# Kernel tuning notes

Hardware: AMD Instinct MI355X
Metric: run time of the kernel (lower is better)

Reference implementation:

```python
import jax, jax.numpy as jnp
import numpy as np

T, B, D, H = 2048, 8, 1024, 1024

def setup_inputs() -> dict:
    key = jax.random.key(0)
    k1, k2, k3 = jax.random.split(key, 3)
    std = 1.0 / H ** 0.5
    return {
        "x": jax.random.normal(k1, (T, B, D), dtype=jnp.float32),
        "h0": jnp.zeros((B, H), dtype=jnp.float32),
        "W_delta": jax.random.uniform(k2, (H, D), dtype=jnp.float32, minval=-0.1 * std, maxval=0.1 * std),
        "b_delta": jnp.full((H,), -1.8, dtype=jnp.float32),
        "W_B": jax.random.uniform(k3, (H, D), dtype=jnp.float32, minval=-std, maxval=std),
        "b_B": jnp.zeros((H,), dtype=jnp.float32),
    }

def reference(x, h0, W_delta, b_delta, W_B, b_B):
    # Projections over all T*B tokens at once (large GEMMs)
    delta = jax.nn.softplus(jnp.einsum('tbd,hd->tbh', x, W_delta) + b_delta)  # [T,B,H]
    decay = jnp.exp(-delta)                                                   # in (0,1)
    Bx = jnp.einsum('tbd,hd->tbh', x, W_B) + b_B                              # [T,B,H]
    # Sequential selective-decay linear recurrence: h = decay*h + (1-decay)*Bx
    def step(h, inp):
        a, bx = inp
        h_new = a * h + (1.0 - a) * bx
        return h_new, h_new
    _, hs = jax.lax.scan(step, h0, (decay, Bx))
    return hs  # [T,B,H]
```

## Files before the change

kernel.cpp:

```cpp
#include <hip/hip_runtime.h>
#include <hip/hip_bf16.h>

#define T_DIM 2048
#define B_DIM 8
#define D_DIM 1024
#define H_DIM 1024
#define M_DIM (T_DIM * B_DIM)
#define NCH (B_DIM * H_DIM)
#define CHUNK 64
#define NCHUNK (T_DIM / CHUNK)
#define NCH2 (NCH / 2)

typedef __bf16 bf16x8 __attribute__((ext_vector_type(8)));
typedef unsigned short us8 __attribute__((ext_vector_type(8)));
typedef float f32x4 __attribute__((ext_vector_type(4)));

__device__ __forceinline__ unsigned short f2bf(float f) {
    unsigned u = __float_as_uint(f);
    u += 0x7fffu + ((u >> 16) & 1u);
    return (unsigned short)(u >> 16);
}
__device__ __forceinline__ float bflo(unsigned u) { return __uint_as_float(u << 16); }
__device__ __forceinline__ float bfhi(unsigned u) { return __uint_as_float(u & 0xffff0000u); }

#define XCELLS  (M_DIM * D_DIM / 8)
#define WCELLS  (H_DIM * D_DIM / 8)
__global__ __launch_bounds__(256) void convert_kernel(
    const float* __restrict__ x, const float* __restrict__ Wd,
    const float* __restrict__ Wb, unsigned short* __restrict__ xb,
    unsigned short* __restrict__ wdb, unsigned short* __restrict__ wbb)
{
    size_t cell = (size_t)blockIdx.x * 256 + threadIdx.x;
    const float* src; unsigned short* dst;
    if (cell < XCELLS)               { src = x  + cell * 8;                    dst = xb  + cell * 8; }
    else if (cell < XCELLS + WCELLS) { size_t c = cell - XCELLS;  src = Wd + c * 8; dst = wdb + c * 8; }
    else                             { size_t c = cell - XCELLS - WCELLS; src = Wb + c * 8; dst = wbb + c * 8; }
    float4 f0 = *(const float4*)src;
    float4 f1 = *(const float4*)(src + 4);
    us8 u;
    u[0]=f2bf(f0.x); u[1]=f2bf(f0.y); u[2]=f2bf(f0.z); u[3]=f2bf(f0.w);
    u[4]=f2bf(f1.x); u[5]=f2bf(f1.y); u[6]=f2bf(f1.z); u[7]=f2bf(f1.w);
    *(us8*)dst = u;
}

__global__ __launch_bounds__(512, 2) void proj_kernel(
    const unsigned short* __restrict__ xb, const unsigned short* __restrict__ wdb,
    const unsigned short* __restrict__ wbb, const float* __restrict__ bd,
    const float* __restrict__ bb, unsigned int* __restrict__ db)
{
    __shared__ us8 lds[2][3072];

    const int tid  = threadIdx.x;
    const int lane = tid & 63;
    const int wid  = tid >> 6;
    const int wm = wid >> 2, wn = wid & 3;
    const int bRow = blockIdx.x * 128;
    const int bCol = blockIdx.y * 128;

    f32x4 accD[4][2], accB[4][2];
    #pragma unroll
    for (int i = 0; i < 4; ++i)
        #pragma unroll
        for (int j = 0; j < 2; ++j) { accD[i][j] = (f32x4)0.0f; accB[i][j] = (f32x4)0.0f; }

    const unsigned short* aBase  = xb  + (size_t)bRow * D_DIM;
    const unsigned short* b0Base = wdb + (size_t)bCol * D_DIM;
    const unsigned short* b1Base = wbb + (size_t)bCol * D_DIM;

    auto stage = [&](int buf, int kt) {
        #pragma unroll
        for (int p = 0; p < 6; ++p) {
            const unsigned short* base = (p < 2) ? aBase : (p < 4 ? b0Base : b1Base);
            int woff = (p & 1) * 512 + wid * 64;
            int w    = woff + lane;
            int row  = w >> 3;
            int kc   = (w & 7) ^ (row & 7);
            __builtin_amdgcn_global_load_lds(
                (const __attribute__((address_space(1))) unsigned int*)
                    (base + (size_t)row * D_DIM + kt + kc * 8),
                (__attribute__((address_space(3))) unsigned int*)
                    (&lds[buf][(p >> 1) * 1024 + woff]),
                16, 0, 0);
        }
    };

    auto compute = [&](int buf) {
        #pragma unroll
        for (int ks = 0; ks < 2; ++ks) {
            const int kc = ks * 4 + (lane >> 4);
            const int sl = kc ^ (lane & 7);
            bf16x8 aF[4], b0F[2], b1F[2];
            #pragma unroll
            for (int mt = 0; mt < 4; ++mt) {
                int r = wm * 64 + mt * 16 + (lane & 15);
                aF[mt] = __builtin_bit_cast(bf16x8, lds[buf][r * 8 + sl]);
            }
            #pragma unroll
            for (int nt = 0; nt < 2; ++nt) {
                int c = wn * 32 + nt * 16 + (lane & 15);
                b0F[nt] = __builtin_bit_cast(bf16x8, lds[buf][1024 + c * 8 + sl]);
                b1F[nt] = __builtin_bit_cast(bf16x8, lds[buf][2048 + c * 8 + sl]);
            }
            #pragma unroll
            for (int nt = 0; nt < 2; ++nt)
                #pragma unroll
                for (int mt = 0; mt < 4; ++mt) {
                    accD[mt][nt] = __builtin_amdgcn_mfma_f32_16x16x32_bf16(aF[mt], b0F[nt], accD[mt][nt], 0, 0, 0);
                    accB[mt][nt] = __builtin_amdgcn_mfma_f32_16x16x32_bf16(aF[mt], b1F[nt], accB[mt][nt], 0, 0, 0);
                }
        }
    };

    stage(0, 0);
    __syncthreads();
    for (int t = 0; t < 15; ++t) {
        stage((t + 1) & 1, (t + 1) * 64);
        compute(t & 1);
        __syncthreads();
    }
    compute(1);

    #pragma unroll
    for (int nt = 0; nt < 2; ++nt) {
        int c = bCol + wn * 32 + nt * 16 + (lane & 15);
        float bdv = bd[c], bbv = bb[c];
        #pragma unroll
        for (int mt = 0; mt < 4; ++mt) {
            int r0 = bRow + wm * 64 + mt * 16 + ((lane >> 4) << 2);
            #pragma unroll
            for (int reg = 0; reg < 4; ++reg) {
                float z  = accD[mt][nt][reg] + bdv;
                float dk = 1.0f / (1.0f + __expf(z));
                float bx = accB[mt][nt][reg] + bbv;
                db[(size_t)(r0 + reg) * H_DIM + c] =
                    (unsigned)f2bf(dk) | ((unsigned)f2bf(bx) << 16);
            }
        }
    }
}

__global__ __launch_bounds__(256) void scan_reduce(
    const uint2* __restrict__ db2, float2* __restrict__ cA, float2* __restrict__ cB)
{
    int c2 = blockIdx.y * 256 + threadIdx.x;
    int i  = blockIdx.x;
    const uint2* p = db2 + (size_t)i * CHUNK * NCH2 + c2;
    float A0 = 1.0f, B0 = 0.0f, A1 = 1.0f, B1 = 0.0f;
    for (int t = 0; t < CHUNK; ++t) {
        uint2 u = p[(size_t)t * NCH2];
        float a0 = bflo(u.x), bx0 = bfhi(u.x);
        float a1 = bflo(u.y), bx1 = bfhi(u.y);
        A0 *= a0; B0 = a0 * B0 + (1.0f - a0) * bx0;
        A1 *= a1; B1 = a1 * B1 + (1.0f - a1) * bx1;
    }
    cA[i * NCH2 + c2] = make_float2(A0, A1);
    cB[i * NCH2 + c2] = make_float2(B0, B1);
}

__global__ __launch_bounds__(256) void scan_chunks(
    const float2* __restrict__ cA, const float2* __restrict__ cB,
    const float2* __restrict__ h0, float2* __restrict__ hstart)
{
    int c2 = blockIdx.x * 256 + threadIdx.x;
    float2 h = h0[c2];
    #pragma unroll
    for (int i = 0; i < NCHUNK; ++i) {
        hstart[i * NCH2 + c2] = h;
        float2 a = cA[i * NCH2 + c2];
        float2 b = cB[i * NCH2 + c2];
        h.x = a.x * h.x + b.x;
        h.y = a.y * h.y + b.y;
    }
}

__global__ __launch_bounds__(256) void scan_apply(
    const uint2* __restrict__ db2, const float2* __restrict__ hstart,
    float2* __restrict__ out2)
{
    int c2 = blockIdx.y * 256 + threadIdx.x;
    int i  = blockIdx.x;
    float2 h = hstart[i * NCH2 + c2];
    const uint2* p = db2 + (size_t)i * CHUNK * NCH2 + c2;
    float2*      o = out2 + (size_t)i * CHUNK * NCH2 + c2;
    for (int t = 0; t < CHUNK; ++t) {
        uint2 u = p[(size_t)t * NCH2];
        float a0 = bflo(u.x), bx0 = bfhi(u.x);
        float a1 = bflo(u.y), bx1 = bfhi(u.y);
        h.x = a0 * h.x + (1.0f - a0) * bx0;
        h.y = a1 * h.y + (1.0f - a1) * bx1;
        o[(size_t)t * NCH2] = h;
    }
}

extern "C" void kernel_launch(void* const* d_in, const int* in_sizes, int n_in,
                              void* d_out, int out_size, void* d_ws, size_t ws_size,
                              hipStream_t stream) {
    const float* x  = (const float*)d_in[0];
    const float* h0 = (const float*)d_in[1];
    const float* Wd = (const float*)d_in[2];
    const float* bd = (const float*)d_in[3];
    const float* Wb = (const float*)d_in[4];
    const float* bb = (const float*)d_in[5];
    float* out = (float*)d_out;

    char* ws = (char*)d_ws;
    unsigned int* db = (unsigned int*)ws;
    float* hstart = (float*)(ws + (size_t)M_DIM * H_DIM * 4);

    char* ob = (char*)d_out;
    unsigned short* xb  = (unsigned short*)ob;
    unsigned short* wdb = (unsigned short*)(ob + ((size_t)32 << 20));
    unsigned short* wbb = (unsigned short*)(ob + ((size_t)34 << 20));
    float* cA = (float*)(ob + ((size_t)36 << 20));
    float* cB = (float*)(ob + ((size_t)37 << 20));

    convert_kernel<<<(XCELLS + 2 * WCELLS) / 256, 256, 0, stream>>>(x, Wd, Wb, xb, wdb, wbb);

    dim3 gProj(M_DIM / 128, H_DIM / 128);
    proj_kernel<<<gProj, 512, 0, stream>>>(xb, wdb, wbb, bd, bb, db);

    scan_reduce<<<dim3(NCHUNK, NCH2 / 256), 256, 0, stream>>>((const uint2*)db, (float2*)cA, (float2*)cB);
    scan_chunks<<<NCH2 / 256, 256, 0, stream>>>((const float2*)cA, (const float2*)cB, (const float2*)h0, (float2*)hstart);
    scan_apply<<<dim3(NCHUNK, NCH2 / 256), 256, 0, stream>>>((const uint2*)db, (const float2*)hstart, (float2*)out);
}
```

Measured before the change: 241.8 us.

## Enlarge GEMM block to 256 rows and fold chunk-carry scan into apply

The projection kernel now uses 1024-thread blocks covering 256 rows of x per block, so each weight tile loaded into LDS is reused across twice as many rows, which cuts global weight traffic. The separate scan_chunks kernel is removed. Each scan_apply block instead recomputes its starting state by walking the preceding chunk carries, which saves one launch and the hstart round trip. In exchange, the redundant carry walk grows with the chunk index. Occupancy also drops to one large block per CU, and the cA/cB buffers move into the workspace.

```diff
diff --git a/kernel.cpp b/kernel.cpp
--- a/kernel.cpp
+++ b/kernel.cpp
@@ -43,18 +43,18 @@
     *(us8*)dst = u;
 }
 
-__global__ __launch_bounds__(512, 2) void proj_kernel(
+__global__ __launch_bounds__(1024, 1) void proj_kernel(
     const unsigned short* __restrict__ xb, const unsigned short* __restrict__ wdb,
     const unsigned short* __restrict__ wbb, const float* __restrict__ bd,
     const float* __restrict__ bb, unsigned int* __restrict__ db)
 {
-    __shared__ us8 lds[2][3072];
+    __shared__ us8 lds[2][4096];
 
     const int tid  = threadIdx.x;
     const int lane = tid & 63;
     const int wid  = tid >> 6;
     const int wm = wid >> 2, wn = wid & 3;
-    const int bRow = blockIdx.x * 128;
+    const int bRow = blockIdx.x * 256;
     const int bCol = blockIdx.y * 128;
 
     f32x4 accD[4][2], accB[4][2];
@@ -69,9 +69,10 @@
 
     auto stage = [&](int buf, int kt) {
         #pragma unroll
-        for (int p = 0; p < 6; ++p) {
-            const unsigned short* base = (p < 2) ? aBase : (p < 4 ? b0Base : b1Base);
-            int woff = (p & 1) * 512 + wid * 64;
+        for (int p = 0; p < 4; ++p) {
+            const unsigned short* base = (p < 2) ? aBase : (p == 2 ? b0Base : b1Base);
+            int tileOff = (p < 2) ? 0 : (p == 2 ? 2048 : 3072);
+            int woff = ((p < 2) ? p * 1024 : 0) + wid * 64;
             int w    = woff + lane;
             int row  = w >> 3;
             int kc   = (w & 7) ^ (row & 7);
@@ -79,7 +80,7 @@
                 (const __attribute__((address_space(1))) unsigned int*)
                     (base + (size_t)row * D_DIM + kt + kc * 8),
                 (__attribute__((address_space(3))) unsigned int*)
-                    (&lds[buf][(p >> 1) * 1024 + woff]),
+                    (&lds[buf][tileOff + woff]),
                 16, 0, 0);
         }
     };
@@ -98,8 +99,8 @@
             #pragma unroll
             for (int nt = 0; nt < 2; ++nt) {
                 int c = wn * 32 + nt * 16 + (lane & 15);
-                b0F[nt] = __builtin_bit_cast(bf16x8, lds[buf][1024 + c * 8 + sl]);
-                b1F[nt] = __builtin_bit_cast(bf16x8, lds[buf][2048 + c * 8 + sl]);
+                b0F[nt] = __builtin_bit_cast(bf16x8, lds[buf][2048 + c * 8 + sl]);
+                b1F[nt] = __builtin_bit_cast(bf16x8, lds[buf][3072 + c * 8 + sl]);
             }
             #pragma unroll
             for (int nt = 0; nt < 2; ++nt)
@@ -157,29 +158,20 @@
     cB[i * NCH2 + c2] = make_float2(B0, B1);
 }
 
-__global__ __launch_bounds__(256) void scan_chunks(
-    const float2* __restrict__ cA, const float2* __restrict__ cB,
-    const float2* __restrict__ h0, float2* __restrict__ hstart)
-{
-    int c2 = blockIdx.x * 256 + threadIdx.x;
+__global__ __launch_bounds__(256) void scan_apply(
+    const uint2* __restrict__ db2, const float2* __restrict__ cA,
+    const float2* __restrict__ cB, const float2* __restrict__ h0,
+    float2* __restrict__ out2)
+{
+    int c2 = blockIdx.y * 256 + threadIdx.x;
+    int i  = blockIdx.x;
     float2 h = h0[c2];
-    #pragma unroll
-    for (int i = 0; i < NCHUNK; ++i) {
-        hstart[i * NCH2 + c2] = h;
-        float2 a = cA[i * NCH2 + c2];
-        float2 b = cB[i * NCH2 + c2];
+    for (int j = 0; j < i; ++j) {
+        float2 a = cA[j * NCH2 + c2];
+        float2 b = cB[j * NCH2 + c2];
         h.x = a.x * h.x + b.x;
         h.y = a.y * h.y + b.y;
     }
-}
-
-__global__ __launch_bounds__(256) void scan_apply(
-    const uint2* __restrict__ db2, const float2* __restrict__ hstart,
-    float2* __restrict__ out2)
-{
-    int c2 = blockIdx.y * 256 + threadIdx.x;
-    int i  = blockIdx.x;
-    float2 h = hstart[i * NCH2 + c2];
     const uint2* p = db2 + (size_t)i * CHUNK * NCH2 + c2;
     float2*      o = out2 + (size_t)i * CHUNK * NCH2 + c2;
     for (int t = 0; t < CHUNK; ++t) {
@@ -205,21 +197,20 @@
 
     char* ws = (char*)d_ws;
     unsigned int* db = (unsigned int*)ws;
-    float* hstart = (float*)(ws + (size_t)M_DIM * H_DIM * 4);
+    float* cA = (float*)(ws + ((size_t)64 << 20));
+    float* cB = (float*)(ws + ((size_t)65 << 20));
 
     char* ob = (char*)d_out;
     unsigned short* xb  = (unsigned short*)ob;
     unsigned short* wdb = (unsigned short*)(ob + ((size_t)32 << 20));
     unsigned short* wbb = (unsigned short*)(ob + ((size_t)34 << 20));
-    float* cA = (float*)(ob + ((size_t)36 << 20));
-    float* cB = (float*)(ob + ((size_t)37 << 20));
 
     convert_kernel<<<(XCELLS + 2 * WCELLS) / 256, 256, 0, stream>>>(x, Wd, Wb, xb, wdb, wbb);
 
-    dim3 gProj(M_DIM / 128, H_DIM / 128);
-    proj_kernel<<<gProj, 512, 0, stream>>>(xb, wdb, wbb, bd, bb, db);
+    dim3 gProj(M_DIM / 256, H_DIM / 128);
+    proj_kernel<<<gProj, 1024, 0, stream>>>(xb, wdb, wbb, bd, bb, db);
 
     scan_reduce<<<dim3(NCHUNK, NCH2 / 256), 256, 0, stream>>>((const uint2*)db, (float2*)cA, (float2*)cB);
-    scan_chunks<<<NCH2 / 256, 256, 0, stream>>>((const float2*)cA, (const float2*)cB, (const float2*)h0, (float2*)hstart);
-    scan_apply<<<dim3(NCHUNK, NCH2 / 256), 256, 0, stream>>>((const uint2*)db, (const float2*)hstart, (float2*)out);
-}
+    scan_apply<<<dim3(NCHUNK, NCH2 / 256), 256, 0, stream>>>(
+        (const uint2*)db, (const float2*)cA, (const float2*)cB, (const float2*)h0, (float2*)out);
+}
```

New measurement: 221.9 us. 8.2% less time.
